# Kernel optimization log

Measured on AMD Instinct MI355X. Metric: run time of the kernel, lower is better.

## Reference

```python
import jax, jax.numpy as jnp
import numpy as np

B, LQ, LK, D, H = 8, 1024, 1024, 1024, 8
DH = D // H  # per-head dim (att_units // num_heads, and V head dim since V = k)
LN_EPS = 1e-5


def setup_inputs() -> dict:
    key = jax.random.key(0)
    ks = jax.random.split(key, 8)
    s = 1.0 / np.sqrt(D)
    return {
        "q": jax.random.normal(ks[0], (B, LQ, D), dtype=jnp.float32),
        "k": jax.random.normal(ks[1], (B, LK, D), dtype=jnp.float32),
        "Wq": jax.random.normal(ks[2], (D, D), dtype=jnp.float32) * s,
        "bq": jnp.zeros((D,), dtype=jnp.float32),
        "Wk": jax.random.normal(ks[3], (D, D), dtype=jnp.float32) * s,
        "bk": jnp.zeros((D,), dtype=jnp.float32),
        "ln_gamma": jnp.ones((D,), dtype=jnp.float32),
        "ln_beta": jnp.zeros((D,), dtype=jnp.float32),
    }


def _layer_norm(x, gamma, beta):
    mu = jnp.mean(x, axis=-1, keepdims=True)
    var = jnp.mean(jnp.square(x - mu), axis=-1, keepdims=True)
    return (x - mu) * jax.lax.rsqrt(var + LN_EPS) * gamma + beta


def reference(q, k, Wq, bq, Wk, bk, ln_gamma, ln_beta):
    # q: [B, LQ, D], k: [B, LK, D]
    Q = q @ Wq + bq                      # [B, LQ, D]
    K = k @ Wk + bk                      # [B, LK, D]
    V = k                                # V is the raw key input (no projection)
    Qh = Q.reshape(B, LQ, H, DH)         # split(att_units//H, -1)+concat(0) == head reshape
    Kh = K.reshape(B, LK, H, DH)
    Vh = V.reshape(B, LK, H, DH)
    sim = jnp.einsum("bqhd,bkhd->bhqk", Qh, Kh) / np.sqrt(DH).astype(np.float32)
    attn = jax.nn.softmax(sim, axis=-1)  # [B, H, LQ, LK]
    att_h = jnp.einsum("bhqk,bkhd->bqhd", attn, Vh).reshape(B, LQ, D)
    att_h = att_h * 0.1 + q * 0.9        # residual blend
    att_h = _layer_norm(att_h, ln_gamma, ln_beta)
    return att_h  # ff_units_list == [] -> ff is None -> ff_h = att_h
```

## Files before the change

### kernel.cpp

```cpp
#include <hip/hip_runtime.h>
#include <hip/hip_bf16.h>
#include <cstdint>

#define BATCH 8
#define SEQ   1024
#define DMODEL 1024
#define NHEAD 8
#define DHEAD 128

using short8 = __attribute__((ext_vector_type(8))) short;
using f32x4  = __attribute__((ext_vector_type(4))) float;
typedef unsigned short u16;

__device__ inline u16 f2bf(float f) {
    union { float f; uint32_t u; } v; v.f = f;
    uint32_t r = (v.u + 0x7FFFu + ((v.u >> 16) & 1u)) >> 16;
    return (u16)r;
}

__device__ inline float exp2_fast(float x) { return __builtin_amdgcn_exp2f(x); }

__device__ inline uint32_t cvtpk_bf16(float a, float b) {
    uint32_t r;
    asm("v_cvt_pk_bf16_f32 %0, %1, %2" : "=v"(r) : "v"(a), "v"(b));
    return r;
}

#define GLL16(g, l)                                                                        \
    __builtin_amdgcn_global_load_lds((__attribute__((address_space(1))) const uint32_t*)(g), \
                                     (__attribute__((address_space(3))) uint32_t*)(l), 16, 0, 0)

__global__ __launch_bounds__(256) void conv_bf16(const float* __restrict__ q,
                                                 u16* __restrict__ dst) {
    size_t e = ((size_t)blockIdx.x * 256 + threadIdx.x) * 8;
    float4 a = *(const float4*)(q + e);
    float4 b = *(const float4*)(q + e + 4);
    uint4 r;
    r.x = cvtpk_bf16(a.x, a.y);
    r.y = cvtpk_bf16(a.z, a.w);
    r.z = cvtpk_bf16(b.x, b.y);
    r.w = cvtpk_bf16(b.z, b.w);
    *(uint4*)(dst + e) = r;
}

__global__ void transpose_conv(const float* __restrict__ Wq,
                               const float* __restrict__ Wk,
                               const float* __restrict__ kin,
                               u16* __restrict__ WqT,
                               u16* __restrict__ WkT,
                               u16* __restrict__ Vt,
                               u16* __restrict__ kb) {
    __shared__ float tile[32][33];
    int z = blockIdx.z;
    const float* src;
    u16* dst;
    u16* sdst = nullptr;
    if (z == 0)      { src = Wq; dst = WqT; }
    else if (z == 1) { src = Wk; dst = WkT; }
    else {
        src  = kin + (size_t)(z - 2) * DMODEL * SEQ;
        dst  = Vt  + (size_t)(z - 2) * DMODEL * SEQ;
        sdst = kb  + (size_t)(z - 2) * DMODEL * SEQ;
    }
    int x  = blockIdx.x * 32 + threadIdx.x;
    int y0 = blockIdx.y * 32;
    for (int i = threadIdx.y; i < 32; i += 8) {
        float v = src[(size_t)(y0 + i) * 1024 + x];
        tile[i][threadIdx.x] = v;
        if (sdst) sdst[(size_t)(y0 + i) * 1024 + x] = f2bf(v);
    }
    __syncthreads();
    int xo  = y0 + threadIdx.x;
    int yo0 = blockIdx.x * 32;
    for (int i = threadIdx.y; i < 32; i += 8)
        dst[(size_t)(yo0 + i) * 1024 + xo] = f2bf(tile[threadIdx.x][i]);
}

__global__ __launch_bounds__(256, 4) void gemm_dual(const u16* __restrict__ Aq,
                                                    const u16* __restrict__ Ak,
                                                    const u16* __restrict__ BTq,
                                                    const u16* __restrict__ BTk,
                                                    const float* __restrict__ biasq,
                                                    const float* __restrict__ biask,
                                                    u16* __restrict__ Outq,
                                                    u16* __restrict__ Outk) {
    __shared__ __align__(16) u16 As[2][128 * 32];
    __shared__ __align__(16) u16 Bs[2][128 * 32];

    int bid = blockIdx.x;
    int half = bid >> 9;
    int b2 = bid & 511;
    const u16* A  = half ? Ak  : Aq;
    const u16* BT = half ? BTk : BTq;
    const float* bias = half ? biask : biasq;
    u16* Out = half ? Outk : Outq;
    float scale = half ? 1.0f : (0.08838834764831845f * 1.4426950408889634f);

    int swz = (b2 & 7) * 64 + (b2 >> 3);
    int mt = swz >> 3, nt = swz & 7;
    int m0 = mt * 128, n0 = nt * 128;

    int t = threadIdx.x, lane = t & 63, w = t >> 6;
    int wm = w >> 1, wn = w & 1;
    int lr = lane & 15, lg = lane >> 4;

    const u16* pa[2];
    const u16* pb[2];
#pragma unroll
    for (int i = 0; i < 2; ++i) {
        int L = (w * 2 + i) * 64 + lane;
        int rp = L >> 3, ss = L & 7;
        int u = ss ^ (rp & 7);
        int row = (rp << 1) | (u >> 2);
        int g = u & 3;
        pa[i] = A  + (size_t)(m0 + row) * 1024 + g * 8;
        pb[i] = BT + (size_t)(n0 + row) * 1024 + g * 8;
    }
    int aoff[4], boff[4];
#pragma unroll
    for (int f = 0; f < 4; ++f) {
        int rowA = wm * 64 + f * 16 + lr;
        int sA = (((rowA & 1) << 2) | lg) ^ ((rowA >> 1) & 7);
        aoff[f] = (rowA >> 1) * 64 + sA * 8;
        int rowB = wn * 64 + f * 16 + lr;
        int sB = (((rowB & 1) << 2) | lg) ^ ((rowB >> 1) & 7);
        boff[f] = (rowB >> 1) * 64 + sB * 8;
    }

    f32x4 acc[4][4] = {};

#define GSTAGE(buf)                                         \
    {                                                       \
        _Pragma("unroll")                                   \
        for (int i = 0; i < 2; ++i) {                       \
            GLL16(pa[i], &As[buf][(w * 2 + i) * 512]);      \
            GLL16(pb[i], &Bs[buf][(w * 2 + i) * 512]);      \
            pa[i] += 32;                                    \
            pb[i] += 32;                                    \
        }                                                   \
    }

    GSTAGE(0);
    __syncthreads();

    int cur = 0;
    for (int k0 = 0; k0 < DMODEL; k0 += 32) {
        if (k0 + 32 < DMODEL) GSTAGE(cur ^ 1);
        short8 af[4], bfr[4];
#pragma unroll
        for (int f = 0; f < 4; ++f) {
            af[f]  = *(const short8*)&As[cur][aoff[f]];
            bfr[f] = *(const short8*)&Bs[cur][boff[f]];
        }
        __builtin_amdgcn_s_setprio(1);
#pragma unroll
        for (int fm = 0; fm < 4; ++fm)
#pragma unroll
            for (int fn = 0; fn < 4; ++fn)
                acc[fm][fn] = __builtin_amdgcn_mfma_f32_16x16x32_bf16(af[fm], bfr[fn], acc[fm][fn], 0, 0, 0);
        __builtin_amdgcn_s_setprio(0);
        __syncthreads();
        cur ^= 1;
    }
#undef GSTAGE

#pragma unroll
    for (int fn = 0; fn < 4; ++fn) {
        int col = n0 + wn * 64 + fn * 16 + lr;
        float bv = bias[col];
#pragma unroll
        for (int fm = 0; fm < 4; ++fm)
#pragma unroll
            for (int j = 0; j < 4; ++j) {
                int row = m0 + wm * 64 + fm * 16 + lg * 4 + j;
                Out[(size_t)row * 1024 + col] = f2bf((acc[fm][fn][j] + bv) * scale);
            }
    }
}

__global__ __launch_bounds__(512, 2) void attn_kernel(const u16* __restrict__ Qb,
                                                      const u16* __restrict__ Kb,
                                                      const u16* __restrict__ Vt,
                                                      float* __restrict__ AO) {
    __shared__ __align__(16) u16 Kbuf[2][64 * 128];
    __shared__ __align__(16) u16 Vbuf[2][128 * 64];
    __shared__ __align__(16) u16 Pl[8][2][16 * 64];

    int bid = blockIdx.x;
    int swz = (bid & 7) * 32 + (bid >> 3);
    int bh  = swz >> 2;
    int qt  = swz & 3;
    int b = bh >> 3, h = bh & 7;
    int q0 = qt * 256;

    int t = threadIdx.x, lane = t & 63, w = t >> 6;
    int lr = lane & 15, lg = lane >> 4;

    short8 qfA[4], qfB[4];
    {
        size_t qa = (size_t)(b * SEQ + q0 + w * 32 + lr) * 1024 + h * DHEAD;
        size_t qbB = qa + (size_t)16 * 1024;
#pragma unroll
        for (int kk = 0; kk < 4; ++kk) {
            qfA[kk] = *(const short8*)&Qb[qa  + kk * 32 + lg * 8];
            qfB[kk] = *(const short8*)&Qb[qbB + kk * 32 + lg * 8];
        }
    }

    float mA = -1e30f, lA = 0.f, mB = -1e30f, lB = 0.f;
    f32x4 oA[8] = {}, oB[8] = {};
    u16* PwA = &Pl[w][0][0];
    u16* PwB = &Pl[w][1][0];
    const int pwrow = lr * 64;
    const int lx = lr & 7;

#define STAGE(nb, kk0)                                                                   \
    {                                                                                    \
        _Pragma("unroll")                                                                \
        for (int i = 0; i < 2; ++i) {                                                    \
            int g = (w * 2 + i) * 64 + lane;                                             \
            int row = g >> 4, cp = g & 15;                                               \
            int c = cp ^ (row & 7);                                                      \
            const u16* src = Kb + ((size_t)(b * SEQ + (kk0) + row) * 1024 + h * 128 + c * 8); \
            GLL16(src, &Kbuf[nb][(w * 2 + i) * 512]);                                    \
        }                                                                                \
        _Pragma("unroll")                                                                \
        for (int i = 0; i < 2; ++i) {                                                    \
            int g = (w * 2 + i) * 64 + lane;                                             \
            int d = g >> 3, cp = g & 7;                                                  \
            int c = cp ^ (d & 7);                                                        \
            const u16* src = Vt + ((size_t)(bh * 128 + d) * 1024 + (kk0) + c * 8);       \
            GLL16(src, &Vbuf[nb][(w * 2 + i) * 512]);                                    \
        }                                                                                \
    }

    STAGE(0, 0);
    __syncthreads();

    int cur = 0;
    for (int k0 = 0; k0 < SEQ; k0 += 64) {
        if (k0 + 64 < SEQ) STAGE(cur ^ 1, k0 + 64);

        const u16* Kc = &Kbuf[cur][0];
        f32x4 sA[4] = {}, sB[4] = {};
        __builtin_amdgcn_s_setprio(1);
#pragma unroll
        for (int fn = 0; fn < 4; ++fn) {
            int krow = (fn * 16 + lr) * 128;
#pragma unroll
            for (int kk = 0; kk < 4; ++kk) {
                short8 kf = *(const short8*)&Kc[krow + (((kk * 4 + lg) ^ lx) << 3)];
                sA[fn] = __builtin_amdgcn_mfma_f32_16x16x32_bf16(kf, qfA[kk], sA[fn], 0, 0, 0);
                sB[fn] = __builtin_amdgcn_mfma_f32_16x16x32_bf16(kf, qfB[kk], sB[fn], 0, 0, 0);
            }
        }
        __builtin_amdgcn_s_setprio(0);

        {
            float pm0 = fmaxf(fmaxf(sA[0][0], sA[0][1]), fmaxf(sA[0][2], sA[0][3]));
            float pm1 = fmaxf(fmaxf(sA[1][0], sA[1][1]), fmaxf(sA[1][2], sA[1][3]));
            float pm2 = fmaxf(fmaxf(sA[2][0], sA[2][1]), fmaxf(sA[2][2], sA[2][3]));
            float pm3 = fmaxf(fmaxf(sA[3][0], sA[3][1]), fmaxf(sA[3][2], sA[3][3]));
            float pmax = fmaxf(fmaxf(pm0, pm1), fmaxf(pm2, pm3));
            if (__any(pmax > mA + 11.5416f)) {
                float rm = pmax;
                rm = fmaxf(rm, __shfl_xor(rm, 16));
                rm = fmaxf(rm, __shfl_xor(rm, 32));
                float mnew = fmaxf(mA, rm);
                float alpha = exp2_fast(mA - mnew);
                mA = mnew;
                lA *= alpha;
#pragma unroll
                for (int db = 0; db < 8; ++db) oA[db] *= alpha;
            }
            float p[4][4];
            float ls0 = 0.f, ls1 = 0.f, ls2 = 0.f, ls3 = 0.f;
#pragma unroll
            for (int j = 0; j < 4; ++j) {
                p[0][j] = exp2_fast(sA[0][j] - mA); ls0 += p[0][j];
                p[1][j] = exp2_fast(sA[1][j] - mA); ls1 += p[1][j];
                p[2][j] = exp2_fast(sA[2][j] - mA); ls2 += p[2][j];
                p[3][j] = exp2_fast(sA[3][j] - mA); ls3 += p[3][j];
            }
            lA += (ls0 + ls1) + (ls2 + ls3);
#pragma unroll
            for (int fn = 0; fn < 4; ++fn) {
                uint2 pk;
                pk.x = cvtpk_bf16(p[fn][0], p[fn][1]);
                pk.y = cvtpk_bf16(p[fn][2], p[fn][3]);
                int idx = pwrow + (((fn * 2 + (lg >> 1)) ^ lx) << 3) + ((lg & 1) << 2);
                *(uint2*)&PwA[idx] = pk;
            }
        }
        {
            float pm0 = fmaxf(fmaxf(sB[0][0], sB[0][1]), fmaxf(sB[0][2], sB[0][3]));
            float pm1 = fmaxf(fmaxf(sB[1][0], sB[1][1]), fmaxf(sB[1][2], sB[1][3]));
            float pm2 = fmaxf(fmaxf(sB[2][0], sB[2][1]), fmaxf(sB[2][2], sB[2][3]));
            float pm3 = fmaxf(fmaxf(sB[3][0], sB[3][1]), fmaxf(sB[3][2], sB[3][3]));
            float pmax = fmaxf(fmaxf(pm0, pm1), fmaxf(pm2, pm3));
            if (__any(pmax > mB + 11.5416f)) {
                float rm = pmax;
                rm = fmaxf(rm, __shfl_xor(rm, 16));
                rm = fmaxf(rm, __shfl_xor(rm, 32));
                float mnew = fmaxf(mB, rm);
                float alpha = exp2_fast(mB - mnew);
                mB = mnew;
                lB *= alpha;
#pragma unroll
                for (int db = 0; db < 8; ++db) oB[db] *= alpha;
            }
            float p[4][4];
            float ls0 = 0.f, ls1 = 0.f, ls2 = 0.f, ls3 = 0.f;
#pragma unroll
            for (int j = 0; j < 4; ++j) {
                p[0][j] = exp2_fast(sB[0][j] - mB); ls0 += p[0][j];
                p[1][j] = exp2_fast(sB[1][j] - mB); ls1 += p[1][j];
                p[2][j] = exp2_fast(sB[2][j] - mB); ls2 += p[2][j];
                p[3][j] = exp2_fast(sB[3][j] - mB); ls3 += p[3][j];
            }
            lB += (ls0 + ls1) + (ls2 + ls3);
#pragma unroll
            for (int fn = 0; fn < 4; ++fn) {
                uint2 pk;
                pk.x = cvtpk_bf16(p[fn][0], p[fn][1]);
                pk.y = cvtpk_bf16(p[fn][2], p[fn][3]);
                int idx = pwrow + (((fn * 2 + (lg >> 1)) ^ lx) << 3) + ((lg & 1) << 2);
                *(uint2*)&PwB[idx] = pk;
            }
        }

        const u16* Vc = &Vbuf[cur][0];
        short8 pfA0 = *(const short8*)&PwA[pwrow + ((lg ^ lx) << 3)];
        short8 pfA1 = *(const short8*)&PwA[pwrow + (((4 + lg) ^ lx) << 3)];
        short8 pfB0 = *(const short8*)&PwB[pwrow + ((lg ^ lx) << 3)];
        short8 pfB1 = *(const short8*)&PwB[pwrow + (((4 + lg) ^ lx) << 3)];
        __builtin_amdgcn_s_setprio(1);
#pragma unroll
        for (int db = 0; db < 8; ++db) {
            int vr = (db * 16 + lr) * 64;
            short8 v0 = *(const short8*)&Vc[vr + ((lg ^ lx) << 3)];
            short8 v1 = *(const short8*)&Vc[vr + (((4 + lg) ^ lx) << 3)];
            oA[db] = __builtin_amdgcn_mfma_f32_16x16x32_bf16(v0, pfA0, oA[db], 0, 0, 0);
            oA[db] = __builtin_amdgcn_mfma_f32_16x16x32_bf16(v1, pfA1, oA[db], 0, 0, 0);
            oB[db] = __builtin_amdgcn_mfma_f32_16x16x32_bf16(v0, pfB0, oB[db], 0, 0, 0);
            oB[db] = __builtin_amdgcn_mfma_f32_16x16x32_bf16(v1, pfB1, oB[db], 0, 0, 0);
        }
        __builtin_amdgcn_s_setprio(0);

        __syncthreads();
        cur ^= 1;
    }

    float ltA = lA;
    ltA += __shfl_xor(ltA, 16);
    ltA += __shfl_xor(ltA, 32);
    float invA = 1.f / ltA;
    float ltB = lB;
    ltB += __shfl_xor(ltB, 16);
    ltB += __shfl_xor(ltB, 32);
    float invB = 1.f / ltB;
    size_t obaseA = (size_t)(b * SEQ + q0 + w * 32 + lr) * 1024 + h * DHEAD + lg * 4;
    size_t obaseB = obaseA + (size_t)16 * 1024;
#pragma unroll
    for (int db = 0; db < 8; ++db) {
        float4 ov;
        ov.x = oA[db][0] * invA;
        ov.y = oA[db][1] * invA;
        ov.z = oA[db][2] * invA;
        ov.w = oA[db][3] * invA;
        *(float4*)&AO[obaseA + db * 16] = ov;
        float4 ow;
        ow.x = oB[db][0] * invB;
        ow.y = oB[db][1] * invB;
        ow.z = oB[db][2] * invB;
        ow.w = oB[db][3] * invB;
        *(float4*)&AO[obaseB + db * 16] = ow;
    }
#undef STAGE
}

__global__ __launch_bounds__(256) void ln_kernel(float* __restrict__ AO,
                                                 const float* __restrict__ qin,
                                                 const float* __restrict__ gamma,
                                                 const float* __restrict__ beta,
                                                 float* __restrict__ out) {
    __shared__ float red[8];
    int row = blockIdx.x;
    int t = threadIdx.x;
    size_t base = (size_t)row * 1024 + t * 4;

    float4 a = *(const float4*)&AO[base];
    float4 qq = *(const float4*)&qin[base];
    float x0 = a.x * 0.1f + qq.x * 0.9f;
    float x1 = a.y * 0.1f + qq.y * 0.9f;
    float x2 = a.z * 0.1f + qq.z * 0.9f;
    float x3 = a.w * 0.1f + qq.w * 0.9f;

    float s  = x0 + x1 + x2 + x3;
    float s2 = x0 * x0 + x1 * x1 + x2 * x2 + x3 * x3;
    for (int d = 1; d < 64; d <<= 1) {
        s  += __shfl_xor(s, d);
        s2 += __shfl_xor(s2, d);
    }
    int w = t >> 6, lane = t & 63;
    if (lane == 0) { red[w] = s; red[4 + w] = s2; }
    __syncthreads();
    s  = red[0] + red[1] + red[2] + red[3];
    s2 = red[4] + red[5] + red[6] + red[7];

    float mu   = s * (1.f / 1024.f);
    float var  = s2 * (1.f / 1024.f) - mu * mu;
    float rstd = rsqrtf(var + 1e-5f);

    float4 g  = *(const float4*)&gamma[t * 4];
    float4 be = *(const float4*)&beta[t * 4];
    float4 o;
    o.x = (x0 - mu) * rstd * g.x + be.x;
    o.y = (x1 - mu) * rstd * g.y + be.y;
    o.z = (x2 - mu) * rstd * g.z + be.z;
    o.w = (x3 - mu) * rstd * g.w + be.w;
    *(float4*)&out[base] = o;
}

extern "C" void kernel_launch(void* const* d_in, const int* in_sizes, int n_in,
                              void* d_out, int out_size, void* d_ws, size_t ws_size,
                              hipStream_t stream) {
    const float* q     = (const float*)d_in[0];
    const float* k     = (const float*)d_in[1];
    const float* Wq    = (const float*)d_in[2];
    const float* bq    = (const float*)d_in[3];
    const float* Wk    = (const float*)d_in[4];
    const float* bk    = (const float*)d_in[5];
    const float* gamma = (const float*)d_in[6];
    const float* beta  = (const float*)d_in[7];
    float* out = (float*)d_out;

    char* ws = (char*)d_ws;
    u16* WqT = (u16*)ws;
    u16* WkT = (u16*)(ws + (size_t)(2  << 20));
    u16* Qb  = (u16*)(ws + (size_t)(4  << 20));
    u16* Kb  = (u16*)(ws + (size_t)(20 << 20));
    u16* Vt  = (u16*)(ws + (size_t)(36 << 20));

    u16* qb = (u16*)d_out;
    u16* kb = qb + (size_t)8 * 1024 * 1024;

    conv_bf16<<<4096, 256, 0, stream>>>(q, qb);

    transpose_conv<<<dim3(32, 32, 2 + BATCH), dim3(32, 8), 0, stream>>>(Wq, Wk, k, WqT, WkT, Vt, kb);

    gemm_dual<<<1024, 256, 0, stream>>>(qb, kb, WqT, WkT, bq, bk, Qb, Kb);

    attn_kernel<<<256, 512, 0, stream>>>(Qb, Kb, Vt, out);

    ln_kernel<<<8192, 256, 0, stream>>>(out, q, gamma, beta, out);
}
```

Before: 132.7 us.

## Enlarge projection GEMM tiles to 256x256 with 8 waves and staged prefetch

```diff
diff --git a/kernel.cpp b/kernel.cpp
--- a/kernel.cpp
+++ b/kernel.cpp
@@ -76,7 +76,7 @@
         dst[(size_t)(yo0 + i) * 1024 + xo] = f2bf(tile[threadIdx.x][i]);
 }
 
-__global__ __launch_bounds__(256, 4) void gemm_dual(const u16* __restrict__ Aq,
+__global__ __launch_bounds__(512, 2) void gemm_dual(const u16* __restrict__ Aq,
                                                     const u16* __restrict__ Ak,
                                                     const u16* __restrict__ BTq,
                                                     const u16* __restrict__ BTk,
@@ -84,95 +84,115 @@
                                                     const float* __restrict__ biask,
                                                     u16* __restrict__ Outq,
                                                     u16* __restrict__ Outk) {
-    __shared__ __align__(16) u16 As[2][128 * 32];
-    __shared__ __align__(16) u16 Bs[2][128 * 32];
+    __shared__ __align__(16) u16 As[2][2][128 * 64];
+    __shared__ __align__(16) u16 Bs[2][2][128 * 64];
 
     int bid = blockIdx.x;
-    int half = bid >> 9;
-    int b2 = bid & 511;
-    const u16* A  = half ? Ak  : Aq;
-    const u16* BT = half ? BTk : BTq;
-    const float* bias = half ? biask : biasq;
-    u16* Out = half ? Outk : Outq;
-    float scale = half ? 1.0f : (0.08838834764831845f * 1.4426950408889634f);
-
-    int swz = (b2 & 7) * 64 + (b2 >> 3);
-    int mt = swz >> 3, nt = swz & 7;
-    int m0 = mt * 128, n0 = nt * 128;
+    int prj = bid >> 7;
+    int b2 = bid & 127;
+    const u16* A  = prj ? Ak  : Aq;
+    const u16* BT = prj ? BTk : BTq;
+    const float* bias = prj ? biask : biasq;
+    u16* Out = prj ? Outk : Outq;
+    float scale = prj ? 1.0f : (0.08838834764831845f * 1.4426950408889634f);
+
+    int swz = (b2 & 7) * 16 + (b2 >> 3);
+    int mt = swz >> 2, nt = swz & 3;
+    int m0 = mt * 256, n0 = nt * 256;
 
     int t = threadIdx.x, lane = t & 63, w = t >> 6;
-    int wm = w >> 1, wn = w & 1;
+    int wm = w >> 2, wn = w & 3;
     int lr = lane & 15, lg = lane >> 4;
 
-    const u16* pa[2];
-    const u16* pb[2];
+    int rS[2], cS[2], ldsS[2];
 #pragma unroll
     for (int i = 0; i < 2; ++i) {
-        int L = (w * 2 + i) * 64 + lane;
-        int rp = L >> 3, ss = L & 7;
-        int u = ss ^ (rp & 7);
-        int row = (rp << 1) | (u >> 2);
-        int g = u & 3;
-        pa[i] = A  + (size_t)(m0 + row) * 1024 + g * 8;
-        pb[i] = BT + (size_t)(n0 + row) * 1024 + g * 8;
-    }
-    int aoff[4], boff[4];
-#pragma unroll
-    for (int f = 0; f < 4; ++f) {
-        int rowA = wm * 64 + f * 16 + lr;
-        int sA = (((rowA & 1) << 2) | lg) ^ ((rowA >> 1) & 7);
-        aoff[f] = (rowA >> 1) * 64 + sA * 8;
-        int rowB = wn * 64 + f * 16 + lr;
-        int sB = (((rowB & 1) << 2) | lg) ^ ((rowB >> 1) & 7);
-        boff[f] = (rowB >> 1) * 64 + sB * 8;
-    }
-
-    f32x4 acc[4][4] = {};
-
-#define GSTAGE(buf)                                         \
-    {                                                       \
-        _Pragma("unroll")                                   \
-        for (int i = 0; i < 2; ++i) {                       \
-            GLL16(pa[i], &As[buf][(w * 2 + i) * 512]);      \
-            GLL16(pb[i], &Bs[buf][(w * 2 + i) * 512]);      \
-            pa[i] += 32;                                    \
-            pb[i] += 32;                                    \
-        }                                                   \
-    }
-
-    GSTAGE(0);
-    __syncthreads();
-
-    int cur = 0;
-    for (int k0 = 0; k0 < DMODEL; k0 += 32) {
-        if (k0 + 32 < DMODEL) GSTAGE(cur ^ 1);
-        short8 af[4], bfr[4];
-#pragma unroll
-        for (int f = 0; f < 4; ++f) {
-            af[f]  = *(const short8*)&As[cur][aoff[f]];
-            bfr[f] = *(const short8*)&Bs[cur][boff[f]];
-        }
-        __builtin_amdgcn_s_setprio(1);
-#pragma unroll
-        for (int fm = 0; fm < 4; ++fm)
-#pragma unroll
-            for (int fn = 0; fn < 4; ++fn)
-                acc[fm][fn] = __builtin_amdgcn_mfma_f32_16x16x32_bf16(af[fm], bfr[fn], acc[fm][fn], 0, 0, 0);
-        __builtin_amdgcn_s_setprio(0);
-        __syncthreads();
-        cur ^= 1;
-    }
-#undef GSTAGE
+        int L = i * 512 + t;
+        rS[i] = L >> 3;
+        cS[i] = ((L & 7) ^ (rS[i] & 7)) * 8;
+        ldsS[i] = (i * 512 + w * 64) * 8;
+    }
+    int acol[2];
+#pragma unroll
+    for (int ks = 0; ks < 2; ++ks)
+        acol[ks] = ((ks * 4 + lg) ^ (lr & 7)) * 8;
+
+#define STG_A(buf, h, kt)                                                                       \
+    {                                                                                           \
+        GLL16(A + (size_t)(m0 + (h) * 128 + rS[0]) * 1024 + (kt) * 64 + cS[0], &As[buf][h][ldsS[0]]); \
+        GLL16(A + (size_t)(m0 + (h) * 128 + rS[1]) * 1024 + (kt) * 64 + cS[1], &As[buf][h][ldsS[1]]); \
+    }
+#define STG_B(buf, h, kt)                                                                       \
+    {                                                                                           \
+        GLL16(BT + (size_t)(n0 + (h) * 128 + rS[0]) * 1024 + (kt) * 64 + cS[0], &Bs[buf][h][ldsS[0]]); \
+        GLL16(BT + (size_t)(n0 + (h) * 128 + rS[1]) * 1024 + (kt) * 64 + cS[1], &Bs[buf][h][ldsS[1]]); \
+    }
+
+    f32x4 acc[8][4] = {};
+    short8 af[4][2];
+
+    STG_A(0, 0, 0); STG_A(0, 1, 0); STG_B(0, 0, 0); STG_B(0, 1, 0);
+    STG_A(1, 0, 1);
+
+    for (int kt = 0; kt < 16; ++kt) {
+        int buf = kt & 1;
+        if (kt == 15) { asm volatile("s_waitcnt vmcnt(0)" ::: "memory"); }
+        else          { asm volatile("s_waitcnt vmcnt(2)" ::: "memory"); }
+        __builtin_amdgcn_sched_barrier(0);
+        __builtin_amdgcn_s_barrier();
+        __builtin_amdgcn_sched_barrier(0);
+
+#pragma unroll
+        for (int q = 0; q < 4; ++q) {
+            const int fmb = (q >> 1) * 4;
+            const int fnb = (q & 1) * 2;
+            if ((q & 1) == 0) {
+#pragma unroll
+                for (int f = 0; f < 4; ++f)
+#pragma unroll
+                    for (int ks = 0; ks < 2; ++ks)
+                        af[f][ks] = *(const short8*)&As[buf][wm][((fmb + f) * 16 + lr) * 64 + acol[ks]];
+            }
+            short8 bf2[2][2];
+#pragma unroll
+            for (int f = 0; f < 2; ++f)
+#pragma unroll
+                for (int ks = 0; ks < 2; ++ks)
+                    bf2[f][ks] = *(const short8*)&Bs[buf][wn >> 1][((wn & 1) * 64 + (fnb + f) * 16 + lr) * 64 + acol[ks]];
+
+            if (q == 0 && kt + 1 < 16) STG_A(buf ^ 1, 1, kt + 1);
+            if (q == 1 && kt + 1 < 16) STG_B(buf ^ 1, 0, kt + 1);
+            if (q == 2 && kt + 1 < 16) STG_B(buf ^ 1, 1, kt + 1);
+            if (q == 3 && kt + 2 < 16) STG_A(buf, 0, kt + 2);
+
+            __builtin_amdgcn_s_barrier();
+            __builtin_amdgcn_sched_barrier(0);
+            __builtin_amdgcn_s_setprio(1);
+#pragma unroll
+            for (int f = 0; f < 4; ++f)
+#pragma unroll
+                for (int g2 = 0; g2 < 2; ++g2)
+#pragma unroll
+                    for (int ks = 0; ks < 2; ++ks)
+                        acc[fmb + f][fnb + g2] = __builtin_amdgcn_mfma_f32_16x16x32_bf16(
+                            af[f][ks], bf2[g2][ks], acc[fmb + f][fnb + g2], 0, 0, 0);
+            __builtin_amdgcn_s_setprio(0);
+            __builtin_amdgcn_s_barrier();
+            __builtin_amdgcn_sched_barrier(0);
+        }
+    }
+#undef STG_A
+#undef STG_B
 
 #pragma unroll
     for (int fn = 0; fn < 4; ++fn) {
         int col = n0 + wn * 64 + fn * 16 + lr;
         float bv = bias[col];
 #pragma unroll
-        for (int fm = 0; fm < 4; ++fm)
+        for (int fm = 0; fm < 8; ++fm)
 #pragma unroll
             for (int j = 0; j < 4; ++j) {
-                int row = m0 + wm * 64 + fm * 16 + lg * 4 + j;
+                int row = m0 + wm * 128 + fm * 16 + lg * 4 + j;
                 Out[(size_t)row * 1024 + col] = f2bf((acc[fm][fn][j] + bv) * scale);
             }
     }
@@ -449,7 +469,7 @@
 
     transpose_conv<<<dim3(32, 32, 2 + BATCH), dim3(32, 8), 0, stream>>>(Wq, Wk, k, WqT, WkT, Vt, kb);
 
-    gemm_dual<<<1024, 256, 0, stream>>>(qb, kb, WqT, WkT, bq, bk, Qb, Kb);
+    gemm_dual<<<256, 512, 0, stream>>>(qb, kb, WqT, WkT, bq, bk, Qb, Kb);
 
     attn_kernel<<<256, 512, 0, stream>>>(Qb, Kb, Vt, out);
 
```

Result: slower. 136.1 us (+2.5%).

## Fuse q bf16 conversion into transpose kernel and store attention output as bf16

Applied to the files above, without the earlier changes.

```diff
diff --git a/kernel.cpp b/kernel.cpp
--- a/kernel.cpp
+++ b/kernel.cpp
@@ -30,37 +30,31 @@
     __builtin_amdgcn_global_load_lds((__attribute__((address_space(1))) const uint32_t*)(g), \
                                      (__attribute__((address_space(3))) uint32_t*)(l), 16, 0, 0)
 
-__global__ __launch_bounds__(256) void conv_bf16(const float* __restrict__ q,
-                                                 u16* __restrict__ dst) {
-    size_t e = ((size_t)blockIdx.x * 256 + threadIdx.x) * 8;
-    float4 a = *(const float4*)(q + e);
-    float4 b = *(const float4*)(q + e + 4);
-    uint4 r;
-    r.x = cvtpk_bf16(a.x, a.y);
-    r.y = cvtpk_bf16(a.z, a.w);
-    r.z = cvtpk_bf16(b.x, b.y);
-    r.w = cvtpk_bf16(b.z, b.w);
-    *(uint4*)(dst + e) = r;
-}
-
 __global__ void transpose_conv(const float* __restrict__ Wq,
                                const float* __restrict__ Wk,
                                const float* __restrict__ kin,
+                               const float* __restrict__ qin,
                                u16* __restrict__ WqT,
                                u16* __restrict__ WkT,
                                u16* __restrict__ Vt,
-                               u16* __restrict__ kb) {
+                               u16* __restrict__ kb,
+                               u16* __restrict__ qb) {
     __shared__ float tile[32][33];
     int z = blockIdx.z;
     const float* src;
     u16* dst;
     u16* sdst = nullptr;
+    const float* qsrc = nullptr;
+    u16* qdst = nullptr;
     if (z == 0)      { src = Wq; dst = WqT; }
     else if (z == 1) { src = Wk; dst = WkT; }
     else {
-        src  = kin + (size_t)(z - 2) * DMODEL * SEQ;
-        dst  = Vt  + (size_t)(z - 2) * DMODEL * SEQ;
-        sdst = kb  + (size_t)(z - 2) * DMODEL * SEQ;
+        size_t off = (size_t)(z - 2) * DMODEL * SEQ;
+        src  = kin + off;
+        dst  = Vt  + off;
+        sdst = kb  + off;
+        qsrc = qin + off;
+        qdst = qb  + off;
     }
     int x  = blockIdx.x * 32 + threadIdx.x;
     int y0 = blockIdx.y * 32;
@@ -68,6 +62,10 @@
         float v = src[(size_t)(y0 + i) * 1024 + x];
         tile[i][threadIdx.x] = v;
         if (sdst) sdst[(size_t)(y0 + i) * 1024 + x] = f2bf(v);
+    }
+    if (qsrc) {
+        for (int i = threadIdx.y; i < 32; i += 8)
+            qdst[(size_t)(y0 + i) * 1024 + x] = f2bf(qsrc[(size_t)(y0 + i) * 1024 + x]);
     }
     __syncthreads();
     int xo  = y0 + threadIdx.x;
@@ -181,7 +179,8 @@
 __global__ __launch_bounds__(512, 2) void attn_kernel(const u16* __restrict__ Qb,
                                                       const u16* __restrict__ Kb,
                                                       const u16* __restrict__ Vt,
-                                                      float* __restrict__ AO) {
+                                                      float* __restrict__ AO,
+                                                      u16* __restrict__ AOb) {
     __shared__ __align__(16) u16 Kbuf[2][64 * 128];
     __shared__ __align__(16) u16 Vbuf[2][128 * 64];
     __shared__ __align__(16) u16 Pl[8][2][16 * 64];
@@ -361,25 +360,39 @@
     float invB = 1.f / ltB;
     size_t obaseA = (size_t)(b * SEQ + q0 + w * 32 + lr) * 1024 + h * DHEAD + lg * 4;
     size_t obaseB = obaseA + (size_t)16 * 1024;
-#pragma unroll
-    for (int db = 0; db < 8; ++db) {
-        float4 ov;
-        ov.x = oA[db][0] * invA;
-        ov.y = oA[db][1] * invA;
-        ov.z = oA[db][2] * invA;
-        ov.w = oA[db][3] * invA;
-        *(float4*)&AO[obaseA + db * 16] = ov;
-        float4 ow;
-        ow.x = oB[db][0] * invB;
-        ow.y = oB[db][1] * invB;
-        ow.z = oB[db][2] * invB;
-        ow.w = oB[db][3] * invB;
-        *(float4*)&AO[obaseB + db * 16] = ow;
+    if (AOb) {
+#pragma unroll
+        for (int db = 0; db < 8; ++db) {
+            uint2 pa, pb2;
+            pa.x = cvtpk_bf16(oA[db][0] * invA, oA[db][1] * invA);
+            pa.y = cvtpk_bf16(oA[db][2] * invA, oA[db][3] * invA);
+            pb2.x = cvtpk_bf16(oB[db][0] * invB, oB[db][1] * invB);
+            pb2.y = cvtpk_bf16(oB[db][2] * invB, oB[db][3] * invB);
+            *(uint2*)&AOb[obaseA + db * 16] = pa;
+            *(uint2*)&AOb[obaseB + db * 16] = pb2;
+        }
+    } else {
+#pragma unroll
+        for (int db = 0; db < 8; ++db) {
+            float4 ov;
+            ov.x = oA[db][0] * invA;
+            ov.y = oA[db][1] * invA;
+            ov.z = oA[db][2] * invA;
+            ov.w = oA[db][3] * invA;
+            *(float4*)&AO[obaseA + db * 16] = ov;
+            float4 ow;
+            ow.x = oB[db][0] * invB;
+            ow.y = oB[db][1] * invB;
+            ow.z = oB[db][2] * invB;
+            ow.w = oB[db][3] * invB;
+            *(float4*)&AO[obaseB + db * 16] = ow;
+        }
     }
 #undef STAGE
 }
 
-__global__ __launch_bounds__(256) void ln_kernel(float* __restrict__ AO,
+__global__ __launch_bounds__(256) void ln_kernel(const float* __restrict__ AOf,
+                                                 const u16* __restrict__ AOb,
                                                  const float* __restrict__ qin,
                                                  const float* __restrict__ gamma,
                                                  const float* __restrict__ beta,
@@ -389,12 +402,22 @@
     int t = threadIdx.x;
     size_t base = (size_t)row * 1024 + t * 4;
 
-    float4 a = *(const float4*)&AO[base];
+    float a0, a1, a2, a3;
+    if (AOb) {
+        ushort4 u = *(const ushort4*)&AOb[base];
+        union { uint32_t i; float f; } c0, c1, c2, c3;
+        c0.i = (uint32_t)u.x << 16; c1.i = (uint32_t)u.y << 16;
+        c2.i = (uint32_t)u.z << 16; c3.i = (uint32_t)u.w << 16;
+        a0 = c0.f; a1 = c1.f; a2 = c2.f; a3 = c3.f;
+    } else {
+        float4 a = *(const float4*)&AOf[base];
+        a0 = a.x; a1 = a.y; a2 = a.z; a3 = a.w;
+    }
     float4 qq = *(const float4*)&qin[base];
-    float x0 = a.x * 0.1f + qq.x * 0.9f;
-    float x1 = a.y * 0.1f + qq.y * 0.9f;
-    float x2 = a.z * 0.1f + qq.z * 0.9f;
-    float x3 = a.w * 0.1f + qq.w * 0.9f;
+    float x0 = a0 * 0.1f + qq.x * 0.9f;
+    float x1 = a1 * 0.1f + qq.y * 0.9f;
+    float x2 = a2 * 0.1f + qq.z * 0.9f;
+    float x3 = a3 * 0.1f + qq.w * 0.9f;
 
     float s  = x0 + x1 + x2 + x3;
     float s2 = x0 * x0 + x1 * x1 + x2 * x2 + x3 * x3;
@@ -441,17 +464,16 @@
     u16* Qb  = (u16*)(ws + (size_t)(4  << 20));
     u16* Kb  = (u16*)(ws + (size_t)(20 << 20));
     u16* Vt  = (u16*)(ws + (size_t)(36 << 20));
+    u16* AOb = (ws_size >= ((size_t)68 << 20)) ? (u16*)(ws + ((size_t)52 << 20)) : nullptr;
 
     u16* qb = (u16*)d_out;
     u16* kb = qb + (size_t)8 * 1024 * 1024;
 
-    conv_bf16<<<4096, 256, 0, stream>>>(q, qb);
-
-    transpose_conv<<<dim3(32, 32, 2 + BATCH), dim3(32, 8), 0, stream>>>(Wq, Wk, k, WqT, WkT, Vt, kb);
+    transpose_conv<<<dim3(32, 32, 2 + BATCH), dim3(32, 8), 0, stream>>>(Wq, Wk, k, q, WqT, WkT, Vt, kb, qb);
 
     gemm_dual<<<1024, 256, 0, stream>>>(qb, kb, WqT, WkT, bq, bk, Qb, Kb);
 
-    attn_kernel<<<256, 512, 0, stream>>>(Qb, Kb, Vt, out);
-
-    ln_kernel<<<8192, 256, 0, stream>>>(out, q, gamma, beta, out);
-}
+    attn_kernel<<<256, 512, 0, stream>>>(Qb, Kb, Vt, out, AOb);
+
+    ln_kernel<<<8192, 256, 0, stream>>>(out, AOb, q, gamma, beta, out);
+}
```

After: 128.4 us. -3.3%, faster.
